# Kernel optimization log

Measured on AMD Instinct MI355X. Metric: run time of the kernel, lower is better.

The kernel has to match this reference:

```python
import jax, jax.numpy as jnp
import numpy as np

B, H, W_SP, C = 256, 14, 14, 768
NUM_CLASSES = 701


def setup_inputs() -> dict:
    key = jax.random.key(0)
    k1, k2, k3 = jax.random.split(key, 3)
    x1 = jax.random.normal(k1, (B, H, W_SP, C), dtype=jnp.float32)
    x2 = jax.random.normal(k2, (B, H, W_SP, C), dtype=jnp.float32)
    W = jax.random.normal(k3, (C, NUM_CLASSES), dtype=jnp.float32) * 0.02
    b = jnp.zeros((NUM_CLASSES,), dtype=jnp.float32)
    return {"x1": x1, "x2": x2, "W": W, "b": b}


def _sgm(feats):
    """Vectorized SGM: per-sample sort by normalized token energy, gap-based
    split index, masked means for background/foreground. feats: [B, N, C]."""
    n = feats.shape[1]
    M = feats.sum(axis=-1)                                  # [B, N] token energies
    mn = M.min(axis=-1, keepdims=True)
    mx = M.max(axis=-1, keepdims=True)
    Mn = (M - mn) / (mx - mn)                               # normalized to [0,1]
    order = jnp.argsort(Mn, axis=-1)                        # ascending
    sorted_tens = jnp.take_along_axis(feats, order[:, :, None], axis=1)  # [B,N,C]
    sorted_M = jnp.take_along_axis(Mn, order, axis=-1)      # [B, N]
    # diff[j] = M[j+1]-M[j], forced to 0 where M[j]==0 (as in original)
    diff = jnp.where(sorted_M[:, :-1] == 0.0, 0.0,
                     sorted_M[:, 1:] - sorted_M[:, :-1])    # [B, N-1]
    k = jnp.argmax(diff, axis=-1)                           # [B] split index
    idx = jnp.arange(n)[None, :]                            # [1, N]
    fg_mask = (idx < k[:, None]).astype(feats.dtype)        # rows [:k] -> foreground
    bg_mask = 1.0 - fg_mask                                 # rows [k:] -> background
    fg_cnt = jnp.maximum(k.astype(feats.dtype), 1.0)[:, None]
    bg_cnt = jnp.maximum((n - k).astype(feats.dtype), 1.0)[:, None]
    foregr = jnp.einsum('bnc,bn->bc', sorted_tens, fg_mask) / fg_cnt
    backgr = jnp.einsum('bnc,bn->bc', sorted_tens, bg_mask) / bg_cnt
    return backgr, foregr


def reference(x1, x2, W, b):
    # flatten spatial dims into a token axis: [B, H*W, C]
    f1 = x1.reshape(x1.shape[0], -1, x1.shape[-1])
    f2 = x2.reshape(x2.shape[0], -1, x2.shape[-1])
    x1_bg, x1_fg = _sgm(f1)
    x2_bg, x2_fg = _sgm(f2)
    classif = lambda v: v @ W + b
    return (classif(x1_bg), classif(x1_fg), classif(x2_bg), classif(x2_fg))
```

## Files before the change

kernel.cpp:

```cpp
#include <hip/hip_runtime.h>
#include <hip/hip_bf16.h>

#define NTOK 196
#define CDIM 768
#define BSAMP 256
#define NCLS 701
#define NCLSP 704

typedef __attribute__((ext_vector_type(8))) short bf16x8;
typedef __attribute__((ext_vector_type(4))) float f32x4;

__device__ __forceinline__ void add4(float4& a, const float4& b) {
  a.x += b.x; a.y += b.y; a.z += b.z; a.w += b.w;
}

__global__ __launch_bounds__(512, 4) void sgm_kernel(const float* __restrict__ x1,
                                                     const float* __restrict__ x2,
                                                     __hip_bfloat16* __restrict__ Vb) {
  const int task = blockIdx.x;
  const int s  = task & 255;
  const int br = task >> 8;
  const float* __restrict__ feats = (br ? x2 : x1) + (size_t)s * (NTOK * CDIM);

  const int tid  = threadIdx.x;
  const int lane = tid & 63;
  const int wv   = tid >> 6;

  __shared__ float Msh[NTOK];
  __shared__ float Mn[NTOK];
  __shared__ float sortedv[NTOK];
  __shared__ int   rnk[NTOK];
  __shared__ int   list[NTOK];
  __shared__ float redmin[8], redmax[8];
  __shared__ int   kSh;
  __shared__ int   cntSh;
  __shared__ float partS[8][CDIM];
  __shared__ float partT[8][CDIM];

  float4 acc[3];
  #pragma unroll
  for (int g = 0; g < 3; g++) acc[g] = make_float4(0.f, 0.f, 0.f, 0.f);

  const float* lanebase = feats + lane * 4;

  for (int ib = 0; ib < 4; ib++) {
    const int t0 = wv + ib * 48;
    const float* p = lanebase + (size_t)t0 * CDIM;
    float4 r[6][3];
    #pragma unroll
    for (int j = 0; j < 6; j++)
      #pragma unroll
      for (int g = 0; g < 3; g++)
        r[j][g] = *(const float4*)(p + j * (8 * CDIM) + g * 256);

    float e[6];
    #pragma unroll
    for (int j = 0; j < 6; j++) {
      #pragma unroll
      for (int g = 0; g < 3; g++) add4(acc[g], r[j][g]);
      e[j] = ((r[j][0].x + r[j][0].y) + (r[j][0].z + r[j][0].w))
           + ((r[j][1].x + r[j][1].y) + (r[j][1].z + r[j][1].w))
           + ((r[j][2].x + r[j][2].y) + (r[j][2].z + r[j][2].w));
    }
    #pragma unroll
    for (int off = 32; off; off >>= 1) {
      #pragma unroll
      for (int j = 0; j < 6; j++) e[j] += __shfl_xor(e[j], off);
    }
    if (lane == 0) {
      #pragma unroll
      for (int j = 0; j < 6; j++) Msh[t0 + j * 8] = e[j];
    }
  }
  if (wv < 4) {
    const int t = 192 + wv;
    const float* p = lanebase + (size_t)t * CDIM;
    float4 r0 = *(const float4*)(p);
    float4 r1 = *(const float4*)(p + 256);
    float4 r2 = *(const float4*)(p + 512);
    add4(acc[0], r0); add4(acc[1], r1); add4(acc[2], r2);
    float e = ((r0.x + r0.y) + (r0.z + r0.w))
            + ((r1.x + r1.y) + (r1.z + r1.w))
            + ((r2.x + r2.y) + (r2.z + r2.w));
    #pragma unroll
    for (int off = 32; off; off >>= 1) e += __shfl_xor(e, off);
    if (lane == 0) Msh[t] = e;
  }
  if (tid == 0) cntSh = 0;
  __syncthreads();

  float vmn = (tid < NTOK) ? Msh[tid] :  1e30f;
  float vmx = (tid < NTOK) ? Msh[tid] : -1e30f;
  #pragma unroll
  for (int off = 32; off; off >>= 1) {
    vmn = fminf(vmn, __shfl_xor(vmn, off));
    vmx = fmaxf(vmx, __shfl_xor(vmx, off));
  }
  if (lane == 0) { redmin[wv] = vmn; redmax[wv] = vmx; }
  __syncthreads();
  float mn = redmin[0], mx = redmax[0];
  #pragma unroll
  for (int i = 1; i < 8; i++) { mn = fminf(mn, redmin[i]); mx = fmaxf(mx, redmax[i]); }
  const float rng = mx - mn;
  if (tid < NTOK) Mn[tid] = (Msh[tid] - mn) / rng;
  __syncthreads();

  if (tid < NTOK) {
    const float mv = Mn[tid];
    int r = 0;
    for (int u = 0; u < NTOK; u++) {
      const float o = Mn[u];
      r += (o < mv) || (o == mv && u < tid);
    }
    sortedv[r] = mv;
    rnk[tid] = r;
  }
  __syncthreads();

  if (tid < 64) {
    float bd = -1.0f; int bj = NTOK;
    for (int j = lane; j < NTOK - 1; j += 64) {
      const float sj = sortedv[j];
      const float d = (sj == 0.0f) ? 0.0f : (sortedv[j + 1] - sj);
      if (d > bd || (d == bd && j < bj)) { bd = d; bj = j; }
    }
    #pragma unroll
    for (int off = 32; off; off >>= 1) {
      const float od = __shfl_xor(bd, off);
      const int   oj = __shfl_xor(bj, off);
      if (od > bd || (od == bd && oj < bj)) { bd = od; bj = oj; }
    }
    if (lane == 0) kSh = bj;
  }
  __syncthreads();

  const int k = kSh;
  const bool takeFg = (k <= NTOK / 2);

  if (tid < NTOK) {
    const int r = rnk[tid];
    const bool inSet = takeFg ? (r < k) : (r >= k);
    if (inSet) { int p = atomicAdd(&cntSh, 1); list[p] = tid; }
  }
  __syncthreads();
  const int m = cntSh;

  float4 tacc[3];
  #pragma unroll
  for (int g = 0; g < 3; g++) tacc[g] = make_float4(0.f, 0.f, 0.f, 0.f);

  for (int i0 = wv * 4; i0 < m; i0 += 32) {
    const int nb = m - i0;
    float4 r[4][3];
    #pragma unroll
    for (int j = 0; j < 4; j++) {
      if (j < nb) {
        const int t = list[i0 + j];
        const float* p = lanebase + (size_t)t * CDIM;
        #pragma unroll
        for (int g = 0; g < 3; g++) r[j][g] = *(const float4*)(p + g * 256);
      }
    }
    #pragma unroll
    for (int j = 0; j < 4; j++) {
      if (j < nb) {
        #pragma unroll
        for (int g = 0; g < 3; g++) add4(tacc[g], r[j][g]);
      }
    }
  }

  const int base = lane * 4;
  #pragma unroll
  for (int g = 0; g < 3; g++) {
    *(float4*)&partS[wv][base + g * 256] = acc[g];
    *(float4*)&partT[wv][base + g * 256] = tacc[g];
  }
  __syncthreads();

  const float fgc = (float)(k > 1 ? k : 1);
  const float bgc = (float)((NTOK - k) > 1 ? (NTOK - k) : 1);
  const size_t rowFg = (size_t)(2 * br + 1) * BSAMP + s;
  const size_t rowBg = (size_t)(2 * br    ) * BSAMP + s;
  for (int c = tid; c < CDIM; c += 512) {
    float S = 0.0f, T = 0.0f;
    #pragma unroll
    for (int w = 0; w < 8; w++) { S += partS[w][c]; T += partT[w][c]; }
    float fg, bg;
    if (takeFg) { fg = T;     bg = S - T; }
    else        { bg = T;     fg = S - T; }
    Vb[rowFg * CDIM + c] = __float2bfloat16(fg / fgc);
    Vb[rowBg * CDIM + c] = __float2bfloat16(bg / bgc);
  }
}

__global__ __launch_bounds__(256) void wt_kernel(const float* __restrict__ W,
                                                 __hip_bfloat16* __restrict__ WT) {
  __shared__ float tile[32][33];
  const int c0 = blockIdx.x * 32;
  const int k0 = blockIdx.y * 32;
  const int tx = threadIdx.x & 31;
  const int ty = threadIdx.x >> 5;
  #pragma unroll
  for (int i = 0; i < 4; i++) {
    const int kr = ty + i * 8;
    const int c = c0 + tx;
    tile[kr][tx] = (c < NCLS) ? W[(size_t)(k0 + kr) * NCLS + c] : 0.0f;
  }
  __syncthreads();
  #pragma unroll
  for (int i = 0; i < 4; i++) {
    const int cr = ty + i * 8;
    const int cls = c0 + cr;
    WT[(size_t)cls * CDIM + k0 + tx] = __float2bfloat16(tile[tx][cr]);
  }
}

__global__ __launch_bounds__(256) void mfma_gemm(const __hip_bfloat16* __restrict__ Vb,
                                                 const __hip_bfloat16* __restrict__ WT,
                                                 const float* __restrict__ bias,
                                                 float* __restrict__ out) {
  const int w = blockIdx.x * 4 + (threadIdx.x >> 6);
  const int lane = threadIdx.x & 63;
  const int tr = w / (NCLSP / 16);
  const int tc = w % (NCLSP / 16);
  const int m0 = tr * 16;
  const int n0 = tc * 16;
  const int ko = (lane >> 4) * 8;

  const short* aptr = (const short*)Vb + (size_t)(m0 + (lane & 15)) * CDIM + ko;
  const short* bptr = (const short*)WT + (size_t)(n0 + (lane & 15)) * CDIM + ko;

  f32x4 acc = {0.f, 0.f, 0.f, 0.f};
  #pragma unroll
  for (int k0 = 0; k0 < CDIM; k0 += 32) {
    const bf16x8 af = *(const bf16x8*)(aptr + k0);
    const bf16x8 bf = *(const bf16x8*)(bptr + k0);
    acc = __builtin_amdgcn_mfma_f32_16x16x32_bf16(af, bf, acc, 0, 0, 0);
  }

  const int crow = m0 + (lane >> 4) * 4;
  const int ccol = n0 + (lane & 15);
  if (ccol < NCLS) {
    const float bv = bias[ccol];
    #pragma unroll
    for (int r = 0; r < 4; r++)
      out[(size_t)(crow + r) * NCLS + ccol] = acc[r] + bv;
  }
}

extern "C" void kernel_launch(void* const* d_in, const int* in_sizes, int n_in,
                              void* d_out, int out_size, void* d_ws, size_t ws_size,
                              hipStream_t stream) {
  const float* x1 = (const float*)d_in[0];
  const float* x2 = (const float*)d_in[1];
  const float* W  = (const float*)d_in[2];
  const float* b  = (const float*)d_in[3];
  float* out = (float*)d_out;

  __hip_bfloat16* Vb = (__hip_bfloat16*)d_ws;
  __hip_bfloat16* WT = (__hip_bfloat16*)((char*)d_ws + 1024 * CDIM * 2);

  sgm_kernel<<<512, 512, 0, stream>>>(x1, x2, Vb);
  wt_kernel<<<dim3(22, 24), 256, 0, stream>>>(W, WT);
  mfma_gemm<<<704, 256, 0, stream>>>(Vb, WT, b, out);
}
```

Baseline: 347.1 us.

## Split SGM into chunked column-sum kernel and per-sample finalize kernel

```diff
diff --git a/kernel.cpp b/kernel.cpp
--- a/kernel.cpp
+++ b/kernel.cpp
@@ -4,8 +4,11 @@
 #define NTOK 196
 #define CDIM 768
 #define BSAMP 256
+#define TASKS 512
 #define NCLS 701
 #define NCLSP 704
+#define NCHK 7
+#define CHTOK 28
 
 typedef __attribute__((ext_vector_type(8))) short bf16x8;
 typedef __attribute__((ext_vector_type(4))) float f32x4;
@@ -14,10 +17,13 @@
   a.x += b.x; a.y += b.y; a.z += b.z; a.w += b.w;
 }
 
-__global__ __launch_bounds__(512, 4) void sgm_kernel(const float* __restrict__ x1,
-                                                     const float* __restrict__ x2,
-                                                     __hip_bfloat16* __restrict__ Vb) {
-  const int task = blockIdx.x;
+__global__ __launch_bounds__(256, 8) void colsum_kernel(const float* __restrict__ x1,
+                                                        const float* __restrict__ x2,
+                                                        float* __restrict__ colp,
+                                                        float* __restrict__ Mg) {
+  const int blk   = blockIdx.x;
+  const int task  = blk / NCHK;
+  const int chunk = blk % NCHK;
   const int s  = task & 255;
   const int br = task >> 8;
   const float* __restrict__ feats = (br ? x2 : x1) + (size_t)s * (NTOK * CDIM);
@@ -26,54 +32,44 @@
   const int lane = tid & 63;
   const int wv   = tid >> 6;
 
-  __shared__ float Msh[NTOK];
-  __shared__ float Mn[NTOK];
-  __shared__ float sortedv[NTOK];
-  __shared__ int   rnk[NTOK];
-  __shared__ int   list[NTOK];
-  __shared__ float redmin[8], redmax[8];
-  __shared__ int   kSh;
-  __shared__ int   cntSh;
-  __shared__ float partS[8][CDIM];
-  __shared__ float partT[8][CDIM];
+  __shared__ float part[4][CDIM];
 
   float4 acc[3];
   #pragma unroll
   for (int g = 0; g < 3; g++) acc[g] = make_float4(0.f, 0.f, 0.f, 0.f);
 
   const float* lanebase = feats + lane * 4;
-
-  for (int ib = 0; ib < 4; ib++) {
-    const int t0 = wv + ib * 48;
-    const float* p = lanebase + (size_t)t0 * CDIM;
-    float4 r[6][3];
-    #pragma unroll
-    for (int j = 0; j < 6; j++)
-      #pragma unroll
-      for (int g = 0; g < 3; g++)
-        r[j][g] = *(const float4*)(p + j * (8 * CDIM) + g * 256);
-
-    float e[6];
-    #pragma unroll
-    for (int j = 0; j < 6; j++) {
-      #pragma unroll
-      for (int g = 0; g < 3; g++) add4(acc[g], r[j][g]);
-      e[j] = ((r[j][0].x + r[j][0].y) + (r[j][0].z + r[j][0].w))
-           + ((r[j][1].x + r[j][1].y) + (r[j][1].z + r[j][1].w))
-           + ((r[j][2].x + r[j][2].y) + (r[j][2].z + r[j][2].w));
-    }
+  const int tbase = chunk * CHTOK;
+
+  #pragma unroll 1
+  for (int i = 0; i < 6; i += 2) {
+    const int ta = tbase + wv + 4 * i;
+    const int tb = ta + 4;
+    const float* pa = lanebase + (size_t)ta * CDIM;
+    const float* pb = lanebase + (size_t)tb * CDIM;
+    float4 ra0 = *(const float4*)(pa);
+    float4 ra1 = *(const float4*)(pa + 256);
+    float4 ra2 = *(const float4*)(pa + 512);
+    float4 rb0 = *(const float4*)(pb);
+    float4 rb1 = *(const float4*)(pb + 256);
+    float4 rb2 = *(const float4*)(pb + 512);
+    add4(acc[0], ra0); add4(acc[1], ra1); add4(acc[2], ra2);
+    add4(acc[0], rb0); add4(acc[1], rb1); add4(acc[2], rb2);
+    float ea = ((ra0.x + ra0.y) + (ra0.z + ra0.w))
+             + ((ra1.x + ra1.y) + (ra1.z + ra1.w))
+             + ((ra2.x + ra2.y) + (ra2.z + ra2.w));
+    float eb = ((rb0.x + rb0.y) + (rb0.z + rb0.w))
+             + ((rb1.x + rb1.y) + (rb1.z + rb1.w))
+             + ((rb2.x + rb2.y) + (rb2.z + rb2.w));
     #pragma unroll
     for (int off = 32; off; off >>= 1) {
-      #pragma unroll
-      for (int j = 0; j < 6; j++) e[j] += __shfl_xor(e[j], off);
-    }
-    if (lane == 0) {
-      #pragma unroll
-      for (int j = 0; j < 6; j++) Msh[t0 + j * 8] = e[j];
-    }
-  }
-  if (wv < 4) {
-    const int t = 192 + wv;
+      ea += __shfl_xor(ea, off);
+      eb += __shfl_xor(eb, off);
+    }
+    if (lane == 0) { Mg[task * NTOK + ta] = ea; Mg[task * NTOK + tb] = eb; }
+  }
+  {
+    const int t = tbase + wv + 24;
     const float* p = lanebase + (size_t)t * CDIM;
     float4 r0 = *(const float4*)(p);
     float4 r1 = *(const float4*)(p + 256);
@@ -84,8 +80,48 @@
             + ((r2.x + r2.y) + (r2.z + r2.w));
     #pragma unroll
     for (int off = 32; off; off >>= 1) e += __shfl_xor(e, off);
-    if (lane == 0) Msh[t] = e;
-  }
+    if (lane == 0) Mg[task * NTOK + t] = e;
+  }
+
+  const int base = lane * 4;
+  #pragma unroll
+  for (int g = 0; g < 3; g++)
+    *(float4*)&part[wv][base + g * 256] = acc[g];
+  __syncthreads();
+
+  #pragma unroll
+  for (int q = 0; q < 3; q++) {
+    const int c = tid + 256 * q;
+    const float v = part[0][c] + part[1][c] + part[2][c] + part[3][c];
+    colp[((size_t)task * NCHK + chunk) * CDIM + c] = v;
+  }
+}
+
+__global__ __launch_bounds__(256) void finalize_kernel(const float* __restrict__ x1,
+                                                       const float* __restrict__ x2,
+                                                       const float* __restrict__ colp,
+                                                       const float* __restrict__ Mg,
+                                                       __hip_bfloat16* __restrict__ Vb) {
+  const int task = blockIdx.x;
+  const int s  = task & 255;
+  const int br = task >> 8;
+  const float* __restrict__ feats = (br ? x2 : x1) + (size_t)s * (NTOK * CDIM);
+
+  const int tid  = threadIdx.x;
+  const int lane = tid & 63;
+  const int wv   = tid >> 6;
+
+  __shared__ float Msh[NTOK];
+  __shared__ float Mn[NTOK];
+  __shared__ float sortedv[NTOK];
+  __shared__ int   rnk[NTOK];
+  __shared__ int   list[NTOK];
+  __shared__ float redmin[4], redmax[4];
+  __shared__ int   kSh;
+  __shared__ int   cntSh;
+  __shared__ float partT[4][CDIM];
+
+  if (tid < NTOK) Msh[tid] = Mg[task * NTOK + tid];
   if (tid == 0) cntSh = 0;
   __syncthreads();
 
@@ -100,7 +136,7 @@
   __syncthreads();
   float mn = redmin[0], mx = redmax[0];
   #pragma unroll
-  for (int i = 1; i < 8; i++) { mn = fminf(mn, redmin[i]); mx = fmaxf(mx, redmax[i]); }
+  for (int i = 1; i < 4; i++) { mn = fminf(mn, redmin[i]); mx = fmaxf(mx, redmax[i]); }
   const float rng = mx - mn;
   if (tid < NTOK) Mn[tid] = (Msh[tid] - mn) / rng;
   __syncthreads();
@@ -149,7 +185,8 @@
   #pragma unroll
   for (int g = 0; g < 3; g++) tacc[g] = make_float4(0.f, 0.f, 0.f, 0.f);
 
-  for (int i0 = wv * 4; i0 < m; i0 += 32) {
+  const float* lanebase = feats + lane * 4;
+  for (int i0 = wv * 4; i0 < m; i0 += 16) {
     const int nb = m - i0;
     float4 r[4][3];
     #pragma unroll
@@ -172,20 +209,20 @@
 
   const int base = lane * 4;
   #pragma unroll
-  for (int g = 0; g < 3; g++) {
-    *(float4*)&partS[wv][base + g * 256] = acc[g];
+  for (int g = 0; g < 3; g++)
     *(float4*)&partT[wv][base + g * 256] = tacc[g];
-  }
   __syncthreads();
 
   const float fgc = (float)(k > 1 ? k : 1);
   const float bgc = (float)((NTOK - k) > 1 ? (NTOK - k) : 1);
   const size_t rowFg = (size_t)(2 * br + 1) * BSAMP + s;
   const size_t rowBg = (size_t)(2 * br    ) * BSAMP + s;
-  for (int c = tid; c < CDIM; c += 512) {
-    float S = 0.0f, T = 0.0f;
-    #pragma unroll
-    for (int w = 0; w < 8; w++) { S += partS[w][c]; T += partT[w][c]; }
+  for (int c = tid; c < CDIM; c += 256) {
+    float T = partT[0][c] + partT[1][c] + partT[2][c] + partT[3][c];
+    float S = 0.0f;
+    #pragma unroll
+    for (int ch = 0; ch < NCHK; ch++)
+      S += colp[((size_t)task * NCHK + ch) * CDIM + c];
     float fg, bg;
     if (takeFg) { fg = T;     bg = S - T; }
     else        { bg = T;     fg = S - T; }
@@ -258,10 +295,16 @@
   const float* b  = (const float*)d_in[3];
   float* out = (float*)d_out;
 
+  const size_t VB_BYTES   = (size_t)4 * BSAMP * CDIM * 2;
+  const size_t WT_BYTES   = (size_t)NCLSP * CDIM * 2;
+  const size_t COLP_BYTES = (size_t)TASKS * NCHK * CDIM * 4;
   __hip_bfloat16* Vb = (__hip_bfloat16*)d_ws;
-  __hip_bfloat16* WT = (__hip_bfloat16*)((char*)d_ws + 1024 * CDIM * 2);
-
-  sgm_kernel<<<512, 512, 0, stream>>>(x1, x2, Vb);
+  __hip_bfloat16* WT = (__hip_bfloat16*)((char*)d_ws + VB_BYTES);
+  float* colp = (float*)((char*)d_ws + VB_BYTES + WT_BYTES);
+  float* Mg   = (float*)((char*)d_ws + VB_BYTES + WT_BYTES + COLP_BYTES);
+
+  colsum_kernel<<<TASKS * NCHK, 256, 0, stream>>>(x1, x2, colp, Mg);
+  finalize_kernel<<<TASKS, 256, 0, stream>>>(x1, x2, colp, Mg, Vb);
   wt_kernel<<<dim3(22, 24), 256, 0, stream>>>(W, WT);
   mfma_gemm<<<704, 256, 0, stream>>>(Vb, WT, b, out);
 }
```

Result: no change. 351.8 us (+1.4%).
